# Kernel tuning notes

Measured on AMD Instinct MI355X. Metric: run time of the kernel, lower is better.

The kernel has to match this reference:

```python
import jax, jax.numpy as jnp
import numpy as np

N_NODES = 100000
N_EDGES = 3200000


def setup_inputs() -> dict:
    key = jax.random.key(0)
    k1, k2, k3, k4 = jax.random.split(key, 4)
    x = jax.random.normal(k1, (N_NODES, 128), dtype=jnp.float32)
    edge_index = jax.random.randint(k2, (2, N_EDGES), 0, N_NODES, dtype=jnp.int64)
    W1 = jax.random.normal(k3, (128, 16), dtype=jnp.float32) * 0.1
    b1 = jnp.zeros((16,), dtype=jnp.float32)
    W2 = jax.random.normal(k4, (16, 1), dtype=jnp.float32) * 0.1
    b2 = jnp.zeros((1,), dtype=jnp.float32)
    return {"x": x, "edge_index": edge_index, "W1": W1, "b1": b1, "W2": W2, "b2": b2}


def _gcn_conv(h, row, col, norm, b, n):
    # message = h[src] * norm, scatter-add into dst (PyG source_to_target flow)
    msg = h[row] * norm[:, None]
    out = jax.ops.segment_sum(msg, col, num_segments=n)
    return out + b


def reference(x, edge_index, W1, b1, W2, b2):
    n = x.shape[0]
    loops = jnp.arange(n, dtype=edge_index.dtype)
    # GCN adds self-loops with weight 1
    row = jnp.concatenate([edge_index[0], loops])
    col = jnp.concatenate([edge_index[1], loops])
    ew = jnp.ones(row.shape[0], dtype=x.dtype)
    deg = jax.ops.segment_sum(ew, col, num_segments=n)
    dinv = jnp.where(deg > 0, deg ** -0.5, 0.0).astype(x.dtype)
    norm = dinv[row] * dinv[col]

    h = _gcn_conv(x @ W1, row, col, norm, b1, n)  # [N,16]
    h = jax.nn.relu(h)
    # dropout p=0.2 is identity in eval mode
    h = _gcn_conv(h @ W2, row, col, norm, b2, n)  # [N,1]
    return jax.nn.sigmoid(h).squeeze(-1)  # [N]
```

## Files before the change

### kernel.cpp

```cpp
#include <hip/hip_runtime.h>
#include <hip/hip_fp16.h>
#include <cstdint>


#define F_IN 128
#define F_HID 16
#define PB 1024
#define PT 8192
#define NBMAX 512
#define CAPMAX 16384

__global__ __launch_bounds__(PB) void partition_kernel(
    const int* __restrict__ row, const int* __restrict__ col,
    int* __restrict__ cursor,
    int* __restrict__ ping,
    int capB, int NB, int n_edges) {
    __shared__ int sh_hist[NBMAX];
    __shared__ int sh_scan[NBMAX];
    __shared__ int sh_cur[NBMAX];
    __shared__ int sh_base[NBMAX];
    __shared__ int sh_wsum[16];
    __shared__ int sh_packed[PT];
    __shared__ unsigned short sh_bkt[PT];

    int t = threadIdx.x;
    int lane = t & 63;
    int wv = t >> 6;
    int ntiles = (n_edges + PT - 1) / PT;
    bool vec_ok = ((n_edges & 3) == 0);

    for (int tile = blockIdx.x; tile < ntiles; tile += gridDim.x) {
        int tbase = tile * PT;
        int tcnt = min(PT, n_edges - tbase);

        if (t < NBMAX) sh_hist[t] = 0;
        __syncthreads();

        int e0 = tbase + t * 8;
        int pk[8], bb[8];
        if (vec_ok && e0 + 8 <= n_edges) {
            int4 a0 = *(const int4*)(row + e0);
            int4 a1 = *(const int4*)(row + e0 + 4);
            int4 c0 = *(const int4*)(col + e0);
            int4 c1 = *(const int4*)(col + e0 + 4);
            int rr[8] = {a0.x, a0.y, a0.z, a0.w, a1.x, a1.y, a1.z, a1.w};
            int cc[8] = {c0.x, c0.y, c0.z, c0.w, c1.x, c1.y, c1.z, c1.w};
#pragma unroll
            for (int k = 0; k < 8; k++) {
                bb[k] = cc[k] >> 8;
                pk[k] = rr[k] | ((cc[k] & 255) << 17);
                atomicAdd(&sh_hist[bb[k]], 1);
            }
        } else {
#pragma unroll
            for (int k = 0; k < 8; k++) {
                int e = e0 + k;
                bb[k] = -1;
                if (e < n_edges) {
                    int r = row[e];
                    int c = col[e];
                    bb[k] = c >> 8;
                    pk[k] = r | ((c & 255) << 17);
                    atomicAdd(&sh_hist[bb[k]], 1);
                }
            }
        }
        __syncthreads();

        {
            int v = (t < NBMAX) ? sh_hist[t] : 0;
            int incl = v;
#pragma unroll
            for (int off = 1; off < 64; off <<= 1) {
                int u = __shfl_up(incl, off, 64);
                if (lane >= off) incl += u;
            }
            if (lane == 63) sh_wsum[wv] = incl;
            __syncthreads();
            if (t < 16) {
                int s = sh_wsum[t];
#pragma unroll
                for (int off = 1; off < 16; off <<= 1) {
                    int u = __shfl_up(s, off, 16);
                    if (t >= off) s += u;
                }
                sh_wsum[t] = s;
            }
            __syncthreads();
            int wexcl = (wv > 0) ? sh_wsum[wv - 1] : 0;
            if (t < NBMAX) sh_scan[t] = incl + wexcl;
        }
        __syncthreads();

        if (t < NBMAX) {
            int h = sh_hist[t];
            sh_cur[t] = sh_scan[t] - h;
            sh_base[t] = (h > 0 && t < NB) ? atomicAdd(&cursor[t], h) : 0;
        }
        __syncthreads();

#pragma unroll
        for (int k = 0; k < 8; k++) {
            if (bb[k] >= 0) {
                int p = atomicAdd(&sh_cur[bb[k]], 1);
                sh_packed[p] = pk[k];
                sh_bkt[p] = (unsigned short)bb[k];
            }
        }
        __syncthreads();

#pragma unroll
        for (int k = 0; k < 8; k++) {
            int p = t + k * PB;
            if (p < tcnt) {
                int b = sh_bkt[p];
                int off = p - (sh_scan[b] - sh_hist[b]);
                int gp = sh_base[b] + off;
                if (gp < capB) ping[(size_t)b * capB + gp] = sh_packed[p];
            }
        }
        __syncthreads();
    }
}

__global__ __launch_bounds__(PB) void bucket_sort_kernel(
    const int* __restrict__ cursor, const int* __restrict__ ping,
    int* __restrict__ pong, int* __restrict__ cnt, int* __restrict__ rowptr,
    int capB, int n) {
    __shared__ int hist[256];
    __shared__ int scan_[256];
    __shared__ int cur[256];
    __shared__ int wsum[16];

    int b = blockIdx.x, t = threadIdx.x;
    int lane = t & 63;
    int wv = t >> 6;
    int cb = min(cursor[b], capB);
    const int* src = ping + (size_t)b * capB;
    int* dst = pong + (size_t)b * capB;

    if (t < 256) hist[t] = 0;
    __syncthreads();
    for (int i = t; i < cb; i += PB) {
        atomicAdd(&hist[(src[i] >> 17) & 255], 1);
    }
    __syncthreads();

    {
        int v = (t < 256) ? hist[t] : 0;
        int incl = v;
#pragma unroll
        for (int off = 1; off < 64; off <<= 1) {
            int u = __shfl_up(incl, off, 64);
            if (lane >= off) incl += u;
        }
        if (lane == 63) wsum[wv] = incl;
        __syncthreads();
        if (t < 16) {
            int s = wsum[t];
#pragma unroll
            for (int off = 1; off < 16; off <<= 1) {
                int u = __shfl_up(s, off, 16);
                if (t >= off) s += u;
            }
            wsum[t] = s;
        }
        __syncthreads();
        int wexcl = (wv > 0) ? wsum[wv - 1] : 0;
        if (t < 256) scan_[t] = incl + wexcl;
    }
    __syncthreads();

    if (t < 256) {
        int excl = scan_[t] - hist[t];
        cur[t] = excl;
        int g = b * 256 + t;
        if (g < n) {
            cnt[g] = hist[t];
            rowptr[g] = b * capB + excl;
        }
    }
    __syncthreads();

    for (int i = t; i < cb; i += PB) {
        int v = src[i];
        int p = atomicAdd(&cur[(v >> 17) & 255], 1);
        dst[p] = v & 131071;
    }
}

__global__ __launch_bounds__(256) void gemm1_kernel(const float* __restrict__ x,
                                                    const float* __restrict__ W1,
                                                    const int* __restrict__ cnt,
                                                    __half* __restrict__ h1p, int n) {
    __shared__ float sW[F_IN * F_HID];
    int tid = threadIdx.x;
    for (int i = tid; i < F_IN * F_HID; i += 256) sW[i] = W1[i];
    __syncthreads();

    int node = blockIdx.x * 256 + tid;
    if (node >= n) return;

    const float4* xr = (const float4*)(x + (size_t)node * F_IN);
    float acc[F_HID];
#pragma unroll
    for (int j = 0; j < F_HID; j++) acc[j] = 0.0f;

#pragma unroll 4
    for (int k4 = 0; k4 < F_IN / 4; k4++) {
        float4 xv = xr[k4];
        const float* w0 = &sW[(k4 * 4 + 0) * F_HID];
        const float* w1 = &sW[(k4 * 4 + 1) * F_HID];
        const float* w2 = &sW[(k4 * 4 + 2) * F_HID];
        const float* w3 = &sW[(k4 * 4 + 3) * F_HID];
#pragma unroll
        for (int j = 0; j < F_HID; j++) {
            acc[j] += xv.x * w0[j] + xv.y * w1[j] + xv.z * w2[j] + xv.w * w3[j];
        }
    }

    float d = rsqrtf((float)cnt[node] + 1.0f);
    __half2 hv[8];
#pragma unroll
    for (int j = 0; j < 8; j++) {
        hv[j] = __floats2half2_rn(acc[2 * j] * d, acc[2 * j + 1] * d);
    }
    float4* o4 = (float4*)(h1p + (size_t)node * F_HID);
    o4[0] = *(float4*)&hv[0];
    o4[1] = *(float4*)&hv[4];
}

__global__ __launch_bounds__(256) void gather1_kernel(const int* __restrict__ rowptr,
                                                      const int* __restrict__ cnt,
                                                      const int* __restrict__ eidx,
                                                      const __half* __restrict__ h1p,
                                                      const float* __restrict__ b1,
                                                      const float* __restrict__ W2,
                                                      float* __restrict__ sp, int n) {
    int g = (blockIdx.x * 256 + threadIdx.x) >> 3;
    int l = threadIdx.x & 7;
    if (g >= n) return;
    int start = rowptr[g];
    int end = start + cnt[g];

    float ax = 0.0f, ay = 0.0f;
    for (int base = start; base < end; base += 8) {
        int rem = end - base;
        int e = base + ((l < rem) ? l : 0);
        int r = eidx[e];
        if (rem >= 8) {
#pragma unroll
            for (int m = 0; m < 8; m++) {
                int rm = __shfl(r, m, 8);
                float2 f = __half22float2(*(const __half2*)(h1p + (size_t)rm * F_HID + 2 * l));
                ax += f.x; ay += f.y;
            }
        } else {
            for (int m = 0; m < rem; m++) {
                int rm = __shfl(r, m, 8);
                float2 f = __half22float2(*(const __half2*)(h1p + (size_t)rm * F_HID + 2 * l));
                ax += f.x; ay += f.y;
            }
        }
    }

    float dc = rsqrtf((float)cnt[g] + 1.0f);
    float2 fs = __half22float2(*(const __half2*)(h1p + (size_t)g * F_HID + 2 * l));
    float v0 = (ax + fs.x) * dc + b1[2 * l];
    float v1 = (ay + fs.y) * dc + b1[2 * l + 1];
    v0 = fmaxf(v0, 0.0f);
    v1 = fmaxf(v1, 0.0f);
    float t = v0 * W2[2 * l] + v1 * W2[2 * l + 1];
    t += __shfl_xor(t, 1, 8);
    t += __shfl_xor(t, 2, 8);
    t += __shfl_xor(t, 4, 8);
    if (l == 0) sp[g] = t * dc;
}

__global__ __launch_bounds__(256) void gather2_kernel(const int* __restrict__ rowptr,
                                                      const int* __restrict__ cnt,
                                                      const int* __restrict__ eidx,
                                                      const float* __restrict__ sp,
                                                      const float* __restrict__ b2,
                                                      float* __restrict__ out, int n) {
    int g = (blockIdx.x * 256 + threadIdx.x) >> 4;
    int lane = threadIdx.x & 15;
    if (g >= n) return;
    int start = rowptr[g];
    int end = start + cnt[g];

    float acc = 0.0f;
    for (int e = start + lane; e < end; e += 16) {
        acc += sp[eidx[e]];
    }
    acc += __shfl_xor(acc, 1, 16);
    acc += __shfl_xor(acc, 2, 16);
    acc += __shfl_xor(acc, 4, 16);
    acc += __shfl_xor(acc, 8, 16);
    if (lane == 0) {
        float v = (acc + sp[g]) * rsqrtf((float)cnt[g] + 1.0f) + b2[0];
        out[g] = 1.0f / (1.0f + __expf(-v));
    }
}

__global__ void bucket_scatter_kernel(const int* __restrict__ row,
                                      const int* __restrict__ col,
                                      int* __restrict__ cnt,
                                      int* __restrict__ eidx,
                                      int cap, int n_edges) {
    int e = blockIdx.x * blockDim.x + threadIdx.x;
    if (e < n_edges) {
        int c = col[e];
        int p = atomicAdd(&cnt[c], 1);
        if (p < cap) eidx[(size_t)c * cap + p] = row[e];
    }
}

__global__ __launch_bounds__(256) void gemm1f_kernel(const float* __restrict__ x,
                                                     const float* __restrict__ W1,
                                                     const int* __restrict__ cnt,
                                                     float* __restrict__ h1p, int n) {
    __shared__ float sW[F_IN * F_HID];
    int tid = threadIdx.x;
    for (int i = tid; i < F_IN * F_HID; i += 256) sW[i] = W1[i];
    __syncthreads();
    int node = blockIdx.x * 256 + tid;
    if (node >= n) return;
    const float4* xr = (const float4*)(x + (size_t)node * F_IN);
    float acc[F_HID];
#pragma unroll
    for (int j = 0; j < F_HID; j++) acc[j] = 0.0f;
#pragma unroll 4
    for (int k4 = 0; k4 < F_IN / 4; k4++) {
        float4 xv = xr[k4];
        const float* w0 = &sW[(k4 * 4 + 0) * F_HID];
        const float* w1 = &sW[(k4 * 4 + 1) * F_HID];
        const float* w2 = &sW[(k4 * 4 + 2) * F_HID];
        const float* w3 = &sW[(k4 * 4 + 3) * F_HID];
#pragma unroll
        for (int j = 0; j < F_HID; j++) {
            acc[j] += xv.x * w0[j] + xv.y * w1[j] + xv.z * w2[j] + xv.w * w3[j];
        }
    }
    float d = rsqrtf((float)cnt[node] + 1.0f);
    float4* outp = (float4*)(h1p + (size_t)node * F_HID);
    outp[0] = make_float4(acc[0] * d, acc[1] * d, acc[2] * d, acc[3] * d);
    outp[1] = make_float4(acc[4] * d, acc[5] * d, acc[6] * d, acc[7] * d);
    outp[2] = make_float4(acc[8] * d, acc[9] * d, acc[10] * d, acc[11] * d);
    outp[3] = make_float4(acc[12] * d, acc[13] * d, acc[14] * d, acc[15] * d);
}

__global__ __launch_bounds__(256) void fb_gather1_kernel(const int* __restrict__ cnt,
                                                         const int* __restrict__ eidx,
                                                         const float* __restrict__ h1p,
                                                         const float* __restrict__ b1,
                                                         const float* __restrict__ W2,
                                                         float* __restrict__ sp,
                                                         int cap, int n) {
    int g = (blockIdx.x * 256 + threadIdx.x) >> 4;
    int lane = threadIdx.x & 15;
    if (g >= n) return;
    int start = g * cap;
    int end = start + min(cnt[g], cap);
    float acc = 0.0f;
    for (int base = start; base < end; base += 16) {
        int e = base + lane;
        int r = (e < end) ? eidx[e] : 0;
        int m_cnt = min(16, end - base);
        for (int m = 0; m < m_cnt; m++) {
            int rm = __shfl(r, m, 16);
            acc += h1p[(size_t)rm * F_HID + lane];
        }
    }
    float dc = rsqrtf((float)cnt[g] + 1.0f);
    float v = (acc + h1p[(size_t)g * F_HID + lane]) * dc + b1[lane];
    v = fmaxf(v, 0.0f);
    float t = v * W2[lane];
    t += __shfl_xor(t, 1, 16);
    t += __shfl_xor(t, 2, 16);
    t += __shfl_xor(t, 4, 16);
    t += __shfl_xor(t, 8, 16);
    if (lane == 0) sp[g] = t * dc;
}

__global__ __launch_bounds__(256) void fb_gather2_kernel(const int* __restrict__ cnt,
                                                         const int* __restrict__ eidx,
                                                         const float* __restrict__ sp,
                                                         const float* __restrict__ b2,
                                                         float* __restrict__ out,
                                                         int cap, int n) {
    int g = (blockIdx.x * 256 + threadIdx.x) >> 4;
    int lane = threadIdx.x & 15;
    if (g >= n) return;
    int start = g * cap;
    int end = start + min(cnt[g], cap);
    float acc = 0.0f;
    for (int e = start + lane; e < end; e += 16) {
        acc += sp[eidx[e]];
    }
    acc += __shfl_xor(acc, 1, 16);
    acc += __shfl_xor(acc, 2, 16);
    acc += __shfl_xor(acc, 4, 16);
    acc += __shfl_xor(acc, 8, 16);
    if (lane == 0) {
        float v = (acc + sp[g]) * rsqrtf((float)cnt[g] + 1.0f) + b2[0];
        out[g] = 1.0f / (1.0f + __expf(-v));
    }
}

extern "C" void kernel_launch(void* const* d_in, const int* in_sizes, int n_in,
                              void* d_out, int out_size, void* d_ws, size_t ws_size,
                              hipStream_t stream) {
    const float* x  = (const float*)d_in[0];
    const int*   ei = (const int*)d_in[1];
    const float* W1 = (const float*)d_in[2];
    const float* b1 = (const float*)d_in[3];
    const float* W2 = (const float*)d_in[4];
    const float* b2 = (const float*)d_in[5];
    float* out = (float*)d_out;

    const int n = in_sizes[0] / F_IN;
    const int n_edges = in_sizes[1] / 2;
    const int* row = ei;
    const int* col = ei + n_edges;

    const size_t S = ((size_t)n + 511) & ~(size_t)511;
    const size_t words = ws_size / 4;

    const int B = 256;
    const int gridE = (n_edges + B - 1) / B;
    const int gridN = (n + B - 1) / B;

    const int NB = (n + 255) >> 8;
    int meanB = (NB > 0) ? (n_edges / NB) : 0;
    int capB = ((meanB + meanB / 8 + 1024) + 15) & ~15;
    size_t need_new = 11 * S + (size_t)NBMAX + 2 * (size_t)NB * (size_t)capB;

    if (n <= 131072 && NB <= NBMAX && capB <= CAPMAX && words >= need_new) {
        int*    cnt    = (int*)d_ws;
        int*    rowptr = cnt + S;
        float*  sp     = (float*)(rowptr + S);
        __half* h1p    = (__half*)(sp + S);
        int*    cursor = (int*)((float*)(sp + S) + 8 * S);
        int*    ping   = cursor + NBMAX;
        int*    pong   = ping + (size_t)NB * capB;

        hipMemsetAsync(cursor, 0, NBMAX * sizeof(int), stream);
        int ntiles = (n_edges + PT - 1) / PT;
        int pgrid = min(2048, ntiles);
        partition_kernel<<<pgrid, PB, 0, stream>>>(row, col, cursor, ping,
                                                   capB, NB, n_edges);
        bucket_sort_kernel<<<NB, PB, 0, stream>>>(cursor, ping, pong, cnt,
                                                  rowptr, capB, n);
        gemm1_kernel<<<gridN, B, 0, stream>>>(x, W1, cnt, h1p, n);
        int gridG1 = (n * 8 + B - 1) / B;
        gather1_kernel<<<gridG1, B, 0, stream>>>(rowptr, cnt, pong, h1p, b1, W2,
                                                 sp, n);
        int gridG2 = (n * 16 + B - 1) / B;
        gather2_kernel<<<gridG2, B, 0, stream>>>(rowptr, cnt, pong, sp, b2, out, n);
    } else {
        int*   cnt  = (int*)d_ws;
        float* sp   = (float*)(cnt + S);
        float* h1pf = sp + S;
        int*   eidx = (int*)(h1pf + 16 * S);
        size_t tail_words = (words > 18 * S) ? (words - 18 * S) : 0;
        int cap = (int)min((size_t)96, tail_words / (size_t)(n > 0 ? n : 1));
        const int gridG = (n * 16 + B - 1) / B;

        hipMemsetAsync(cnt, 0, (size_t)n * sizeof(int), stream);
        bucket_scatter_kernel<<<gridE, B, 0, stream>>>(row, col, cnt, eidx, cap, n_edges);
        gemm1f_kernel<<<gridN, B, 0, stream>>>(x, W1, cnt, h1pf, n);
        fb_gather1_kernel<<<gridG, B, 0, stream>>>(cnt, eidx, h1pf, b1, W2, sp, cap, n);
        fb_gather2_kernel<<<gridG, B, 0, stream>>>(cnt, eidx, sp, b2, out, cap, n);
    }
}
```

Baseline: 197.1 us.

## Drop bucket sort pass; aggregate per-bucket with shared-memory atomics

Removes the second-level bucket sort kernel. Per-node degree counts are now computed with global atomics in the partition kernel. The two gather kernels are replaced by per-bucket kernels that stream the coarse-partitioned edges and accumulate into a padded shared-memory tile with atomics, then apply normalization, ReLU/W2 and sigmoid. This saves a full read and write of the edge list and one launch, at the cost of global atomics on cnt and shared-memory float atomic contention. Only NB (~391) blocks are launched for the gathers, which may underfill the GPU.

Result: slower. 610.0 us (+209.4%).

```diff
diff --git a/kernel.cpp b/kernel.cpp
--- a/kernel.cpp
+++ b/kernel.cpp
@@ -9,9 +9,11 @@
 #define PT 8192
 #define NBMAX 512
 #define CAPMAX 16384
+#define ACCS 17
 
 __global__ __launch_bounds__(PB) void partition_kernel(
     const int* __restrict__ row, const int* __restrict__ col,
+    int* __restrict__ cnt,
     int* __restrict__ cursor,
     int* __restrict__ ping,
     int capB, int NB, int n_edges) {
@@ -50,6 +52,7 @@
                 bb[k] = cc[k] >> 8;
                 pk[k] = rr[k] | ((cc[k] & 255) << 17);
                 atomicAdd(&sh_hist[bb[k]], 1);
+                atomicAdd(&cnt[cc[k]], 1);
             }
         } else {
 #pragma unroll
@@ -62,6 +65,7 @@
                     bb[k] = c >> 8;
                     pk[k] = r | ((c & 255) << 17);
                     atomicAdd(&sh_hist[bb[k]], 1);
+                    atomicAdd(&cnt[c], 1);
                 }
             }
         }
@@ -123,72 +127,6 @@
     }
 }
 
-__global__ __launch_bounds__(PB) void bucket_sort_kernel(
-    const int* __restrict__ cursor, const int* __restrict__ ping,
-    int* __restrict__ pong, int* __restrict__ cnt, int* __restrict__ rowptr,
-    int capB, int n) {
-    __shared__ int hist[256];
-    __shared__ int scan_[256];
-    __shared__ int cur[256];
-    __shared__ int wsum[16];
-
-    int b = blockIdx.x, t = threadIdx.x;
-    int lane = t & 63;
-    int wv = t >> 6;
-    int cb = min(cursor[b], capB);
-    const int* src = ping + (size_t)b * capB;
-    int* dst = pong + (size_t)b * capB;
-
-    if (t < 256) hist[t] = 0;
-    __syncthreads();
-    for (int i = t; i < cb; i += PB) {
-        atomicAdd(&hist[(src[i] >> 17) & 255], 1);
-    }
-    __syncthreads();
-
-    {
-        int v = (t < 256) ? hist[t] : 0;
-        int incl = v;
-#pragma unroll
-        for (int off = 1; off < 64; off <<= 1) {
-            int u = __shfl_up(incl, off, 64);
-            if (lane >= off) incl += u;
-        }
-        if (lane == 63) wsum[wv] = incl;
-        __syncthreads();
-        if (t < 16) {
-            int s = wsum[t];
-#pragma unroll
-            for (int off = 1; off < 16; off <<= 1) {
-                int u = __shfl_up(s, off, 16);
-                if (t >= off) s += u;
-            }
-            wsum[t] = s;
-        }
-        __syncthreads();
-        int wexcl = (wv > 0) ? wsum[wv - 1] : 0;
-        if (t < 256) scan_[t] = incl + wexcl;
-    }
-    __syncthreads();
-
-    if (t < 256) {
-        int excl = scan_[t] - hist[t];
-        cur[t] = excl;
-        int g = b * 256 + t;
-        if (g < n) {
-            cnt[g] = hist[t];
-            rowptr[g] = b * capB + excl;
-        }
-    }
-    __syncthreads();
-
-    for (int i = t; i < cb; i += PB) {
-        int v = src[i];
-        int p = atomicAdd(&cur[(v >> 17) & 255], 1);
-        dst[p] = v & 131071;
-    }
-}
-
 __global__ __launch_bounds__(256) void gemm1_kernel(const float* __restrict__ x,
                                                     const float* __restrict__ W1,
                                                     const int* __restrict__ cnt,
@@ -230,76 +168,73 @@
     o4[1] = *(float4*)&hv[4];
 }
 
-__global__ __launch_bounds__(256) void gather1_kernel(const int* __restrict__ rowptr,
-                                                      const int* __restrict__ cnt,
-                                                      const int* __restrict__ eidx,
-                                                      const __half* __restrict__ h1p,
-                                                      const float* __restrict__ b1,
-                                                      const float* __restrict__ W2,
-                                                      float* __restrict__ sp, int n) {
-    int g = (blockIdx.x * 256 + threadIdx.x) >> 3;
-    int l = threadIdx.x & 7;
-    if (g >= n) return;
-    int start = rowptr[g];
-    int end = start + cnt[g];
-
-    float ax = 0.0f, ay = 0.0f;
-    for (int base = start; base < end; base += 8) {
-        int rem = end - base;
-        int e = base + ((l < rem) ? l : 0);
-        int r = eidx[e];
-        if (rem >= 8) {
-#pragma unroll
-            for (int m = 0; m < 8; m++) {
-                int rm = __shfl(r, m, 8);
-                float2 f = __half22float2(*(const __half2*)(h1p + (size_t)rm * F_HID + 2 * l));
-                ax += f.x; ay += f.y;
-            }
-        } else {
-            for (int m = 0; m < rem; m++) {
-                int rm = __shfl(r, m, 8);
-                float2 f = __half22float2(*(const __half2*)(h1p + (size_t)rm * F_HID + 2 * l));
-                ax += f.x; ay += f.y;
-            }
-        }
-    }
-
-    float dc = rsqrtf((float)cnt[g] + 1.0f);
-    float2 fs = __half22float2(*(const __half2*)(h1p + (size_t)g * F_HID + 2 * l));
-    float v0 = (ax + fs.x) * dc + b1[2 * l];
-    float v1 = (ay + fs.y) * dc + b1[2 * l + 1];
-    v0 = fmaxf(v0, 0.0f);
-    v1 = fmaxf(v1, 0.0f);
-    float t = v0 * W2[2 * l] + v1 * W2[2 * l + 1];
-    t += __shfl_xor(t, 1, 8);
-    t += __shfl_xor(t, 2, 8);
-    t += __shfl_xor(t, 4, 8);
-    if (l == 0) sp[g] = t * dc;
-}
-
-__global__ __launch_bounds__(256) void gather2_kernel(const int* __restrict__ rowptr,
-                                                      const int* __restrict__ cnt,
-                                                      const int* __restrict__ eidx,
-                                                      const float* __restrict__ sp,
-                                                      const float* __restrict__ b2,
-                                                      float* __restrict__ out, int n) {
-    int g = (blockIdx.x * 256 + threadIdx.x) >> 4;
-    int lane = threadIdx.x & 15;
-    if (g >= n) return;
-    int start = rowptr[g];
-    int end = start + cnt[g];
-
-    float acc = 0.0f;
-    for (int e = start + lane; e < end; e += 16) {
-        acc += sp[eidx[e]];
-    }
-    acc += __shfl_xor(acc, 1, 16);
-    acc += __shfl_xor(acc, 2, 16);
-    acc += __shfl_xor(acc, 4, 16);
-    acc += __shfl_xor(acc, 8, 16);
-    if (lane == 0) {
-        float v = (acc + sp[g]) * rsqrtf((float)cnt[g] + 1.0f) + b2[0];
-        out[g] = 1.0f / (1.0f + __expf(-v));
+__global__ __launch_bounds__(1024) void gather1_fused(
+    const int* __restrict__ cursor, const int* __restrict__ ping,
+    const int* __restrict__ cnt, const __half* __restrict__ h1p,
+    const float* __restrict__ b1, const float* __restrict__ W2,
+    float* __restrict__ sp, int capB, int n) {
+    __shared__ float acc[256 * ACCS];
+
+    int b = blockIdx.x, t = threadIdx.x;
+    for (int i = t; i < 256 * ACCS; i += 1024) acc[i] = 0.0f;
+    __syncthreads();
+
+    int cb = min(cursor[b], capB);
+    const int* src = ping + (size_t)b * capB;
+    int l = t & 7;
+
+    for (int i = t >> 3; i < cb; i += 128) {
+        int v = src[i];
+        int r = v & 131071;
+        int sub = (v >> 17) & 255;
+        float2 f = __half22float2(*(const __half2*)(h1p + (size_t)r * F_HID + 2 * l));
+        atomicAdd(&acc[sub * ACCS + 2 * l], f.x);
+        atomicAdd(&acc[sub * ACCS + 2 * l + 1], f.y);
+    }
+    __syncthreads();
+
+    for (int j = t >> 3; j < 256; j += 128) {
+        int g = b * 256 + j;
+        if (g < n) {
+            float dc = rsqrtf((float)cnt[g] + 1.0f);
+            float2 fs = __half22float2(*(const __half2*)(h1p + (size_t)g * F_HID + 2 * l));
+            float v0 = (acc[j * ACCS + 2 * l] + fs.x) * dc + b1[2 * l];
+            float v1 = (acc[j * ACCS + 2 * l + 1] + fs.y) * dc + b1[2 * l + 1];
+            v0 = fmaxf(v0, 0.0f);
+            v1 = fmaxf(v1, 0.0f);
+            float tt = v0 * W2[2 * l] + v1 * W2[2 * l + 1];
+            tt += __shfl_xor(tt, 1, 8);
+            tt += __shfl_xor(tt, 2, 8);
+            tt += __shfl_xor(tt, 4, 8);
+            if (l == 0) sp[g] = tt * dc;
+        }
+    }
+}
+
+__global__ __launch_bounds__(1024) void gather2_fused(
+    const int* __restrict__ cursor, const int* __restrict__ ping,
+    const int* __restrict__ cnt, const float* __restrict__ sp,
+    const float* __restrict__ b2, float* __restrict__ out, int capB, int n) {
+    __shared__ float acc[256];
+
+    int b = blockIdx.x, t = threadIdx.x;
+    if (t < 256) acc[t] = 0.0f;
+    __syncthreads();
+
+    int cb = min(cursor[b], capB);
+    const int* src = ping + (size_t)b * capB;
+    for (int i = t; i < cb; i += 1024) {
+        int v = src[i];
+        atomicAdd(&acc[(v >> 17) & 255], sp[v & 131071]);
+    }
+    __syncthreads();
+
+    if (t < 256) {
+        int g = b * 256 + t;
+        if (g < n) {
+            float vv = (acc[t] + sp[g]) * rsqrtf((float)cnt[g] + 1.0f) + b2[0];
+            out[g] = 1.0f / (1.0f + __expf(-vv));
+        }
     }
 }
 
@@ -434,30 +369,25 @@
     const int NB = (n + 255) >> 8;
     int meanB = (NB > 0) ? (n_edges / NB) : 0;
     int capB = ((meanB + meanB / 8 + 1024) + 15) & ~15;
-    size_t need_new = 11 * S + (size_t)NBMAX + 2 * (size_t)NB * (size_t)capB;
+    size_t need_new = 10 * S + (size_t)NBMAX + (size_t)NB * (size_t)capB;
 
     if (n <= 131072 && NB <= NBMAX && capB <= CAPMAX && words >= need_new) {
         int*    cnt    = (int*)d_ws;
-        int*    rowptr = cnt + S;
-        float*  sp     = (float*)(rowptr + S);
+        int*    cursor = cnt + S;
+        float*  sp     = (float*)(cursor + NBMAX);
         __half* h1p    = (__half*)(sp + S);
-        int*    cursor = (int*)((float*)(sp + S) + 8 * S);
-        int*    ping   = cursor + NBMAX;
-        int*    pong   = ping + (size_t)NB * capB;
-
-        hipMemsetAsync(cursor, 0, NBMAX * sizeof(int), stream);
+        int*    ping   = (int*)(sp + S) + 8 * S;
+
+        hipMemsetAsync(cnt, 0, (S + (size_t)NBMAX) * sizeof(int), stream);
         int ntiles = (n_edges + PT - 1) / PT;
         int pgrid = min(2048, ntiles);
-        partition_kernel<<<pgrid, PB, 0, stream>>>(row, col, cursor, ping,
+        partition_kernel<<<pgrid, PB, 0, stream>>>(row, col, cnt, cursor, ping,
                                                    capB, NB, n_edges);
-        bucket_sort_kernel<<<NB, PB, 0, stream>>>(cursor, ping, pong, cnt,
-                                                  rowptr, capB, n);
         gemm1_kernel<<<gridN, B, 0, stream>>>(x, W1, cnt, h1p, n);
-        int gridG1 = (n * 8 + B - 1) / B;
-        gather1_kernel<<<gridG1, B, 0, stream>>>(rowptr, cnt, pong, h1p, b1, W2,
-                                                 sp, n);
-        int gridG2 = (n * 16 + B - 1) / B;
-        gather2_kernel<<<gridG2, B, 0, stream>>>(rowptr, cnt, pong, sp, b2, out, n);
+        gather1_fused<<<NB, PB, 0, stream>>>(cursor, ping, cnt, h1p, b1, W2,
+                                             sp, capB, n);
+        gather2_fused<<<NB, PB, 0, stream>>>(cursor, ping, cnt, sp, b2, out,
+                                             capB, n);
     } else {
         int*   cnt  = (int*)d_ws;
         float* sp   = (float*)(cnt + S);
```

## Fuse bucket sort into first gather kernel using shared-memory sorted edges

Applied to the files above, without the earlier changes.

Removes the separate bucket_sort kernel and has each 256-node bucket block sort its edges into dynamic shared memory, then run the layer-1 gather straight from that shared buffer, while still writing pong for the second gather. Per-node degree counts are now taken with global atomics in the partition kernel, so gemm1 can run before the sort. This saves one launch and the global re-read of sorted indices. In exchange it adds 3.2M global atomics in partition and gives the gather only NB (~391) large blocks, which may reduce parallelism and latency hiding. CAPMAX is lowered so the shared buffer fits.

New measurement: 296.6 us. +50.5%, slower.

```diff
diff --git a/kernel.cpp b/kernel.cpp
--- a/kernel.cpp
+++ b/kernel.cpp
@@ -8,10 +8,11 @@
 #define PB 1024
 #define PT 8192
 #define NBMAX 512
-#define CAPMAX 16384
+#define CAPMAX 15104
 
 __global__ __launch_bounds__(PB) void partition_kernel(
     const int* __restrict__ row, const int* __restrict__ col,
+    int* __restrict__ cnt,
     int* __restrict__ cursor,
     int* __restrict__ ping,
     int capB, int NB, int n_edges) {
@@ -50,6 +51,7 @@
                 bb[k] = cc[k] >> 8;
                 pk[k] = rr[k] | ((cc[k] & 255) << 17);
                 atomicAdd(&sh_hist[bb[k]], 1);
+                atomicAdd(&cnt[cc[k]], 1);
             }
         } else {
 #pragma unroll
@@ -62,6 +64,7 @@
                     bb[k] = c >> 8;
                     pk[k] = r | ((c & 255) << 17);
                     atomicAdd(&sh_hist[bb[k]], 1);
+                    atomicAdd(&cnt[c], 1);
                 }
             }
         }
@@ -123,72 +126,6 @@
     }
 }
 
-__global__ __launch_bounds__(PB) void bucket_sort_kernel(
-    const int* __restrict__ cursor, const int* __restrict__ ping,
-    int* __restrict__ pong, int* __restrict__ cnt, int* __restrict__ rowptr,
-    int capB, int n) {
-    __shared__ int hist[256];
-    __shared__ int scan_[256];
-    __shared__ int cur[256];
-    __shared__ int wsum[16];
-
-    int b = blockIdx.x, t = threadIdx.x;
-    int lane = t & 63;
-    int wv = t >> 6;
-    int cb = min(cursor[b], capB);
-    const int* src = ping + (size_t)b * capB;
-    int* dst = pong + (size_t)b * capB;
-
-    if (t < 256) hist[t] = 0;
-    __syncthreads();
-    for (int i = t; i < cb; i += PB) {
-        atomicAdd(&hist[(src[i] >> 17) & 255], 1);
-    }
-    __syncthreads();
-
-    {
-        int v = (t < 256) ? hist[t] : 0;
-        int incl = v;
-#pragma unroll
-        for (int off = 1; off < 64; off <<= 1) {
-            int u = __shfl_up(incl, off, 64);
-            if (lane >= off) incl += u;
-        }
-        if (lane == 63) wsum[wv] = incl;
-        __syncthreads();
-        if (t < 16) {
-            int s = wsum[t];
-#pragma unroll
-            for (int off = 1; off < 16; off <<= 1) {
-                int u = __shfl_up(s, off, 16);
-                if (t >= off) s += u;
-            }
-            wsum[t] = s;
-        }
-        __syncthreads();
-        int wexcl = (wv > 0) ? wsum[wv - 1] : 0;
-        if (t < 256) scan_[t] = incl + wexcl;
-    }
-    __syncthreads();
-
-    if (t < 256) {
-        int excl = scan_[t] - hist[t];
-        cur[t] = excl;
-        int g = b * 256 + t;
-        if (g < n) {
-            cnt[g] = hist[t];
-            rowptr[g] = b * capB + excl;
-        }
-    }
-    __syncthreads();
-
-    for (int i = t; i < cb; i += PB) {
-        int v = src[i];
-        int p = atomicAdd(&cur[(v >> 17) & 255], 1);
-        dst[p] = v & 131071;
-    }
-}
-
 __global__ __launch_bounds__(256) void gemm1_kernel(const float* __restrict__ x,
                                                     const float* __restrict__ W1,
                                                     const int* __restrict__ cnt,
@@ -230,51 +167,112 @@
     o4[1] = *(float4*)&hv[4];
 }
 
-__global__ __launch_bounds__(256) void gather1_kernel(const int* __restrict__ rowptr,
-                                                      const int* __restrict__ cnt,
-                                                      const int* __restrict__ eidx,
-                                                      const __half* __restrict__ h1p,
-                                                      const float* __restrict__ b1,
-                                                      const float* __restrict__ W2,
-                                                      float* __restrict__ sp, int n) {
-    int g = (blockIdx.x * 256 + threadIdx.x) >> 3;
-    int l = threadIdx.x & 7;
-    if (g >= n) return;
-    int start = rowptr[g];
-    int end = start + cnt[g];
-
-    float ax = 0.0f, ay = 0.0f;
-    for (int base = start; base < end; base += 8) {
-        int rem = end - base;
-        int e = base + ((l < rem) ? l : 0);
-        int r = eidx[e];
-        if (rem >= 8) {
+__global__ __launch_bounds__(PB) void sort_gather1(
+    const int* __restrict__ cursor, const int* __restrict__ ping,
+    const __half* __restrict__ h1p, const float* __restrict__ b1,
+    const float* __restrict__ W2, float* __restrict__ sp,
+    int* __restrict__ pong, int* __restrict__ rowptr,
+    int capB, int n) {
+    extern __shared__ int B[];
+    __shared__ int hist[256];
+    __shared__ int scan_[256];
+    __shared__ int cur[256];
+    __shared__ int wsum[16];
+
+    int b = blockIdx.x, t = threadIdx.x;
+    int lane = t & 63;
+    int wv = t >> 6;
+
+    if (t < 256) hist[t] = 0;
+    __syncthreads();
+
+    int cb = min(cursor[b], capB);
+    const int* src = ping + (size_t)b * capB;
+
+    for (int i = t; i < cb; i += PB) {
+        atomicAdd(&hist[(src[i] >> 17) & 255], 1);
+    }
+    __syncthreads();
+
+    {
+        int v = (t < 256) ? hist[t] : 0;
+        int incl = v;
+#pragma unroll
+        for (int off = 1; off < 64; off <<= 1) {
+            int u = __shfl_up(incl, off, 64);
+            if (lane >= off) incl += u;
+        }
+        if (lane == 63) wsum[wv] = incl;
+        __syncthreads();
+        if (t < 16) {
+            int s = wsum[t];
+#pragma unroll
+            for (int off = 1; off < 16; off <<= 1) {
+                int u = __shfl_up(s, off, 16);
+                if (t >= off) s += u;
+            }
+            wsum[t] = s;
+        }
+        __syncthreads();
+        int wexcl = (wv > 0) ? wsum[wv - 1] : 0;
+        if (t < 256) scan_[t] = incl + wexcl;
+    }
+    __syncthreads();
+
+    if (t < 256) {
+        int excl = scan_[t] - hist[t];
+        cur[t] = excl;
+        int g = b * 256 + t;
+        if (g < n) rowptr[g] = b * capB + excl;
+    }
+    __syncthreads();
+
+    for (int i = t; i < cb; i += PB) {
+        int v = src[i];
+        int p = atomicAdd(&cur[(v >> 17) & 255], 1);
+        B[p] = v & 131071;
+    }
+    __syncthreads();
+
+    for (int i = t; i < cb; i += PB) {
+        pong[(size_t)b * capB + i] = B[i];
+    }
+
+    int l = t & 7;
+    for (int j = t >> 3; j < 256; j += (PB >> 3)) {
+        int g = b * 256 + j;
+        if (g >= n) continue;
+        int h = hist[j];
+        int base = scan_[j] - h;
+        int end = base + h;
+
+        float ax = 0.0f, ay = 0.0f;
+        for (; base + 8 <= end; base += 8) {
 #pragma unroll
             for (int m = 0; m < 8; m++) {
-                int rm = __shfl(r, m, 8);
+                int rm = B[base + m];
                 float2 f = __half22float2(*(const __half2*)(h1p + (size_t)rm * F_HID + 2 * l));
                 ax += f.x; ay += f.y;
             }
-        } else {
-            for (int m = 0; m < rem; m++) {
-                int rm = __shfl(r, m, 8);
-                float2 f = __half22float2(*(const __half2*)(h1p + (size_t)rm * F_HID + 2 * l));
-                ax += f.x; ay += f.y;
-            }
-        }
-    }
-
-    float dc = rsqrtf((float)cnt[g] + 1.0f);
-    float2 fs = __half22float2(*(const __half2*)(h1p + (size_t)g * F_HID + 2 * l));
-    float v0 = (ax + fs.x) * dc + b1[2 * l];
-    float v1 = (ay + fs.y) * dc + b1[2 * l + 1];
-    v0 = fmaxf(v0, 0.0f);
-    v1 = fmaxf(v1, 0.0f);
-    float t = v0 * W2[2 * l] + v1 * W2[2 * l + 1];
-    t += __shfl_xor(t, 1, 8);
-    t += __shfl_xor(t, 2, 8);
-    t += __shfl_xor(t, 4, 8);
-    if (l == 0) sp[g] = t * dc;
+        }
+        for (int m = 0; m < end - base; m++) {
+            int rm = B[base + m];
+            float2 f = __half22float2(*(const __half2*)(h1p + (size_t)rm * F_HID + 2 * l));
+            ax += f.x; ay += f.y;
+        }
+
+        float dc = rsqrtf((float)h + 1.0f);
+        float2 fs = __half22float2(*(const __half2*)(h1p + (size_t)g * F_HID + 2 * l));
+        float v0 = (ax + fs.x) * dc + b1[2 * l];
+        float v1 = (ay + fs.y) * dc + b1[2 * l + 1];
+        v0 = fmaxf(v0, 0.0f);
+        v1 = fmaxf(v1, 0.0f);
+        float tt = v0 * W2[2 * l] + v1 * W2[2 * l + 1];
+        tt += __shfl_xor(tt, 1, 8);
+        tt += __shfl_xor(tt, 2, 8);
+        tt += __shfl_xor(tt, 4, 8);
+        if (l == 0) sp[g] = tt * dc;
+    }
 }
 
 __global__ __launch_bounds__(256) void gather2_kernel(const int* __restrict__ rowptr,
@@ -438,24 +436,21 @@
 
     if (n <= 131072 && NB <= NBMAX && capB <= CAPMAX && words >= need_new) {
         int*    cnt    = (int*)d_ws;
-        int*    rowptr = cnt + S;
+        int*    cursor = cnt + S;
+        int*    rowptr = cursor + NBMAX;
         float*  sp     = (float*)(rowptr + S);
         __half* h1p    = (__half*)(sp + S);
-        int*    cursor = (int*)((float*)(sp + S) + 8 * S);
-        int*    ping   = cursor + NBMAX;
+        int*    ping   = (int*)(sp + S) + 8 * S;
         int*    pong   = ping + (size_t)NB * capB;
 
-        hipMemsetAsync(cursor, 0, NBMAX * sizeof(int), stream);
+        hipMemsetAsync(cnt, 0, (S + (size_t)NBMAX) * sizeof(int), stream);
         int ntiles = (n_edges + PT - 1) / PT;
         int pgrid = min(2048, ntiles);
-        partition_kernel<<<pgrid, PB, 0, stream>>>(row, col, cursor, ping,
+        partition_kernel<<<pgrid, PB, 0, stream>>>(row, col, cnt, cursor, ping,
                                                    capB, NB, n_edges);
-        bucket_sort_kernel<<<NB, PB, 0, stream>>>(cursor, ping, pong, cnt,
-                                                  rowptr, capB, n);
         gemm1_kernel<<<gridN, B, 0, stream>>>(x, W1, cnt, h1p, n);
-        int gridG1 = (n * 8 + B - 1) / B;
-        gather1_kernel<<<gridG1, B, 0, stream>>>(rowptr, cnt, pong, h1p, b1, W2,
-                                                 sp, n);
+        sort_gather1<<<NB, PB, (size_t)capB * sizeof(int), stream>>>(
+            cursor, ping, h1p, b1, W2, sp, pong, rowptr, capB, n);
         int gridG2 = (n * 16 + B - 1) / B;
         gather2_kernel<<<gridG2, B, 0, stream>>>(rowptr, cnt, pong, sp, b2, out, n);
     } else {
```
